# Optimization experiments

Hardware: AMD Instinct MI355X
Metric: run time of the kernel (lower is better)

## Reference

```python
import jax, jax.numpy as jnp
import numpy as np

N = 400000   # nnum_t (tokens)
C = 256      # dim
H = 8        # num_heads
HD = C // H  # head_dim = 32
K = 32       # patch_size
D = 4        # dilation
BLOCK = K * D
NA = ((N + BLOCK - 1) // BLOCK) * BLOCK  # nnum_a (padded length)
SCALE = HD ** -0.5
INVALID = -1000.0


def setup_inputs() -> dict:
    key = jax.random.key(0)
    ks = jax.random.split(key, 8)
    data = jax.random.normal(ks[0], (N, C), dtype=jnp.float32)
    xyz = jax.random.uniform(ks[1], (N, 3), dtype=jnp.float32) * 1024.0
    depth_idx = jnp.sort(jax.random.randint(ks[2], (N,), 0, 8)).astype(jnp.int64)
    Wqkv = jax.random.normal(ks[3], (C, 3 * C), dtype=jnp.float32) * 0.02
    bqkv = jnp.zeros((3 * C,), dtype=jnp.float32)
    Wproj = jax.random.normal(ks[4], (C, C), dtype=jnp.float32) * 0.02
    bproj = jnp.zeros((C,), dtype=jnp.float32)
    freqs = jax.random.normal(ks[5], (H, HD // 2, 3), dtype=jnp.float32) * 0.02
    return {"data": data, "xyz": xyz, "depth_idx": depth_idx,
            "Wqkv": Wqkv, "bqkv": bqkv, "Wproj": Wproj, "bproj": bproj,
            "freqs": freqs}


def _rotate_half(x):
    x1, x2 = jnp.split(x, 2, axis=-1)
    return jnp.concatenate([-x2, x1], axis=-1)


def reference(data, xyz, depth_idx, Wqkv, bqkv, Wproj, bproj, freqs):
    # qkv projection: (N, 3C)
    qkv = data @ Wqkv + bqkv
    qkv = qkv.reshape(N, 3, H, HD)

    # mixed RoPE: per-head learnable frequencies over 3D positions
    theta = jnp.einsum('nd,hfd->nhf', xyz, freqs)          # (N, H, HD/2)
    emb = jnp.concatenate([theta, theta], axis=-1)         # (N, H, HD)
    cos, sin = jnp.cos(emb), jnp.sin(emb)
    q = qkv[:, 0] * cos + _rotate_half(qkv[:, 0]) * sin
    k = qkv[:, 1] * cos + _rotate_half(qkv[:, 1]) * sin
    v = qkv[:, 2]
    qkv = jnp.stack([q, k, v], axis=1).reshape(N, 3 * C)

    # patch_partition: pad tokens to nnum_a
    pad = NA - N
    qkv = jnp.pad(qkv, ((0, pad), (0, 0)))
    max_d = depth_idx.max()
    depth_p = jnp.pad(depth_idx, (0, pad), constant_values=0) 
    if pad > 0:
        depth_p = depth_p.at[N:].set(max_d + 1)

    # dilation reshuffle: (-1, K, D, 3C) -> (-1, D, K, 3C) -> (-1, K, 3C)
    qkv = qkv.reshape(-1, K, D, 3 * C).transpose(0, 2, 1, 3).reshape(-1, K, 3 * C)
    # split heads: (B, H, K, HD) each
    qkv = qkv.reshape(-1, K, 3, H, HD).transpose(2, 0, 3, 1, 4)
    q, k, v = qkv[0], qkv[1], qkv[2]

    # teacher-forcing mask from depth indices (dilated layout, cond='le')
    m = depth_p.reshape(-1, K, D).transpose(0, 2, 1).reshape(-1, K)  # (B, K)
    diff = m[:, :, None] - m[:, None, :]
    mask = jnp.where(diff < 0, INVALID, 0.0).astype(jnp.float32)     # (B, K, K)

    # windowed attention
    scores = jnp.einsum('bhqd,bhkd->bhqk', q, k) * SCALE + mask[:, None]
    attn = jax.nn.softmax(scores, axis=-1)
    out = jnp.einsum('bhqk,bhkd->bhqd', attn, v)           # (B, H, K, HD)
    out = out.transpose(0, 2, 1, 3).reshape(-1, C)

    # reverse dilation reshuffle and unpad
    out = out.reshape(-1, D, K, C).transpose(0, 2, 1, 3).reshape(-1, C)
    out = out[:N]

    # output projection (dropout is identity at p=0 / eval)
    return out @ Wproj + bproj
```

## Files before the change

### kernel.cpp

```cpp
#include <hip/hip_runtime.h>
#include <math.h>


typedef float  float4v __attribute__((ext_vector_type(4)));
typedef short  bf16x8  __attribute__((ext_vector_type(8)));
typedef unsigned short us4 __attribute__((ext_vector_type(4)));

#define SCALE_ 0.17677669529663687f
#define INV2PI 0.15915494309189535f

__device__ __forceinline__ unsigned short f2bf(float x) {
  union { float f; unsigned u; } v; v.f = x;
  unsigned r = v.u + 0x7FFFu + ((v.u >> 16) & 1u);
  return (unsigned short)(r >> 16);
}
__device__ __forceinline__ unsigned pack2bf(float lo, float hi) {
  return (unsigned)f2bf(lo) | ((unsigned)f2bf(hi) << 16);
}
__device__ __forceinline__ float4v mfma16(bf16x8 a, bf16x8 b, float4v c) {
  return __builtin_amdgcn_mfma_f32_16x16x32_bf16(a, b, c, 0, 0, 0);
}
__device__ __forceinline__ int swz(int off) {
  return off ^ (((off >> 9) & 7) << 4);
}

__global__ __launch_bounds__(256) void k_prep(const float* __restrict__ wqkv,
                                              const float* __restrict__ wproj,
                                              unsigned short* __restrict__ wqf,
                                              unsigned short* __restrict__ wp) {
  int tid = blockIdx.x * 256 + threadIdx.x;
  if (tid < 768 * 256) {
    int h  = tid / 24576;
    int r  = tid - h * 24576;
    int mat = r >> 13;
    int r2  = r & 8191;
    int s = r2 >> 10, g = (r2 >> 8) & 3, col = (r2 >> 3) & 31, e = r2 & 7;
    int ci = s * 32 + g * 8 + e;
    int co = mat * 256 + h * 32 + col;
    wqf[tid] = f2bf(wqkv[ci * 768 + co]);
  } else {
    int u = tid - 768 * 256;
    int co = u >> 8, cpos = u & 255;
    int hh = cpos >> 5, ww = cpos & 31;
    int f = (ww & 1) ? 16 + (ww >> 1) : (ww >> 1);
    wp[u] = f2bf(wproj[(hh * 32 + f) * 256 + co]);
  }
}

#define K1_LDS_BYTES 81920

__global__ __launch_bounds__(512, 4) void k_fused(
    const float* __restrict__ data, const float* __restrict__ xyz,
    const int* __restrict__ depth, const float* __restrict__ bqkv,
    const float* __restrict__ freqs, const unsigned short* __restrict__ wqf,
    unsigned short* __restrict__ aout ) {
  extern __shared__ char smem[];
  const int b    = blockIdx.x;
  const int t    = threadIdx.x;
  const int lane = t & 63;
  const int w    = t >> 6;
  const int g    = lane >> 4;
  const int l15  = lane & 15;
  const int d    = w >> 1;
  const int half = w & 1;

  if (t < 128) ((int*)(smem + 78336))[t] =
      depth[b * 128 + ((t & 31) << 2) + (t >> 5)];
  if (t < 384) ((float*)(smem + 78848))[t] = xyz[(size_t)b * 384 + t];
  if (t < 384) ((float*)(smem + 80384))[t] = freqs[t];

  {
    const float* dbase = data + (size_t)b * 32768;
#pragma unroll
    for (int i = 0; i < 16; ++i) {
      const int fidx = i * 512 + t;
      const float4v v4 = *reinterpret_cast<const float4v*>(dbase + fidx * 4);
      us4 pk;
      pk.x = f2bf(v4.x); pk.y = f2bf(v4.y); pk.z = f2bf(v4.z); pk.w = f2bf(v4.w);
      *reinterpret_cast<us4*>(smem + swz(fidx * 8)) = pk;
    }
  }
  __syncthreads();

  bf16x8 areg[8];
#pragma unroll
  for (int s = 0; s < 8; ++s)
    areg[s] = *reinterpret_cast<const bf16x8*>(
        smem + swz((16 * w + l15) * 512 + s * 64 + g * 16));

  float maskf0[4], maskf1[4];
  {
    const int* ML = (const int*)(smem + 78336);
    const int mk0 = ML[32 * d + l15];
    const int mk1 = ML[32 * d + 16 + l15];
#pragma unroll
    for (int rr = 0; rr < 4; ++rr) {
      const int mq = ML[32 * d + 16 * half + 4 * g + rr];
      maskf0[rr] = (mq < mk0) ? -1000.f : 0.f;
      maskf1[rr] = (mq < mk1) ? -1000.f : 0.f;
    }
  }
  bf16x8 ones;
#pragma unroll
  for (int j = 0; j < 8; ++j) ones[j] = (short)0x3F80;

  __syncthreads();

  const int bb = g * 512 + l15 * 16;

#pragma unroll 1
  for (int h = 0; h < 8; ++h) {
    {
      const char* wb = (const char*)wqf + (size_t)h * 49152 + t * 16;
      const bf16x8 s0 = *reinterpret_cast<const bf16x8*>(wb);
      const bf16x8 s1 = *reinterpret_cast<const bf16x8*>(wb + 8192);
      const bf16x8 s2 = *reinterpret_cast<const bf16x8*>(wb + 16384);
      const bf16x8 s3 = *reinterpret_cast<const bf16x8*>(wb + 24576);
      const bf16x8 s4 = *reinterpret_cast<const bf16x8*>(wb + 32768);
      const bf16x8 s5 = *reinterpret_cast<const bf16x8*>(wb + 40960);
      char* wd = smem + t * 16;
      *reinterpret_cast<bf16x8*>(wd)         = s0;
      *reinterpret_cast<bf16x8*>(wd + 8192)  = s1;
      *reinterpret_cast<bf16x8*>(wd + 16384) = s2;
      *reinterpret_cast<bf16x8*>(wd + 24576) = s3;
      *reinterpret_cast<bf16x8*>(wd + 32768) = s4;
      *reinterpret_cast<bf16x8*>(wd + 40960) = s5;
    }
    __syncthreads();

    {
      float4v q0a = {0.f,0.f,0.f,0.f}, q1a = q0a, k0a = q0a, k1a = q0a;
#pragma unroll
      for (int s = 0; s < 8; ++s) {
        const bf16x8 bq0 = *reinterpret_cast<const bf16x8*>(smem + bb + s * 2048);
        const bf16x8 bq1 = *reinterpret_cast<const bf16x8*>(smem + bb + s * 2048 + 256);
        const bf16x8 bk0 = *reinterpret_cast<const bf16x8*>(smem + bb + s * 2048 + 16384);
        const bf16x8 bk1 = *reinterpret_cast<const bf16x8*>(smem + bb + s * 2048 + 16384 + 256);
        q0a = mfma16(areg[s], bq0, q0a);
        q1a = mfma16(areg[s], bq1, q1a);
        k0a = mfma16(areg[s], bk0, k0a);
        k1a = mfma16(areg[s], bk1, k1a);
      }
      const float bq0v = bqkv[h * 32 + l15];
      const float bq1v = bqkv[h * 32 + 16 + l15];
      const float bk0v = bqkv[256 + h * 32 + l15];
      const float bk1v = bqkv[256 + h * 32 + 16 + l15];
      const float* Fp = (const float*)(smem + 80384) + (h * 16 + l15) * 3;
      const float F0 = Fp[0], F1 = Fp[1], F2 = Fp[2];
#pragma unroll
      for (int rr = 0; rr < 4; ++rr) {
        const int row  = 16 * w + 4 * g + rr;
        const int prow = ((row & 3) << 5) | (row >> 2);
        const float* xp = (const float*)(smem + 78848) + row * 3;
        const float th = xp[0] * F0 + xp[1] * F1 + xp[2] * F2;
        float rev = th * INV2PI;
        rev -= floorf(rev);
        const float sn = __builtin_amdgcn_sinf(rev);
        const float cs = __builtin_amdgcn_cosf(rev);
        const float q0 = q0a[rr] + bq0v, q1 = q1a[rr] + bq1v;
        const float k0 = k0a[rr] + bk0v, k1 = k1a[rr] + bk1v;
        *reinterpret_cast<unsigned*>(smem + 49152 + prow * 80 + 4 * l15) =
            pack2bf(q0 * cs - q1 * sn, q1 * cs + q0 * sn);
        *reinterpret_cast<unsigned*>(smem + 59392 + prow * 80 + 4 * l15) =
            pack2bf(k0 * cs - k1 * sn, k1 * cs + k0 * sn);
      }
    }
    {
      float4v v0a = {0.f,0.f,0.f,0.f}, v1a = v0a;
#pragma unroll
      for (int s = 0; s < 8; ++s) {
        const bf16x8 bv0 = *reinterpret_cast<const bf16x8*>(smem + bb + s * 2048 + 32768);
        const bf16x8 bv1 = *reinterpret_cast<const bf16x8*>(smem + bb + s * 2048 + 32768 + 256);
        v0a = mfma16(areg[s], bv0, v0a);
        v1a = mfma16(areg[s], bv1, v1a);
      }
      const float bv0v = bqkv[512 + h * 32 + l15];
      const float bv1v = bqkv[512 + h * 32 + 16 + l15];
#pragma unroll
      for (int rr = 0; rr < 4; ++rr) {
        const int row = 16 * w + 4 * g + rr;
        const int kk = row >> 2, dd = row & 3;
        const int cpos = (kk < 16) ? (kk << 1) : (((kk - 16) << 1) | 1);
        *reinterpret_cast<unsigned short*>(
            smem + 69632 + l15 * 272 + (dd * 32 + cpos) * 2) = f2bf(v0a[rr] + bv0v);
        *reinterpret_cast<unsigned short*>(
            smem + 69632 + (l15 + 16) * 272 + (dd * 32 + cpos) * 2) = f2bf(v1a[rr] + bv1v);
      }
    }
    __syncthreads();

    {
      const bf16x8 aq = *reinterpret_cast<const bf16x8*>(
          smem + 49152 + (32 * d + 16 * half + l15) * 80 + 16 * g);
      const bf16x8 bk0 = *reinterpret_cast<const bf16x8*>(
          smem + 59392 + (32 * d + l15) * 80 + 16 * g);
      const bf16x8 bk1 = *reinterpret_cast<const bf16x8*>(
          smem + 59392 + (32 * d + 16 + l15) * 80 + 16 * g);
      float4v s0 = {0.f,0.f,0.f,0.f}, s1 = s0;
      s0 = mfma16(aq, bk0, s0);
      s1 = mfma16(aq, bk1, s1);

      char* plw = smem + w * 1280;
#pragma unroll
      for (int rr = 0; rr < 4; ++rr) {
        const float p0 = __expf(s0[rr] * SCALE_ + maskf0[rr]);
        const float p1 = __expf(s1[rr] * SCALE_ + maskf1[rr]);
        *reinterpret_cast<unsigned*>(plw + (4 * g + rr) * 80 + 4 * l15) =
            pack2bf(p0, p1);
      }
      const bf16x8 ap = *reinterpret_cast<const bf16x8*>(plw + l15 * 80 + 16 * g);
      const bf16x8 bv0 = *reinterpret_cast<const bf16x8*>(
          smem + 69632 + l15 * 272 + d * 64 + 16 * g);
      const bf16x8 bv1 = *reinterpret_cast<const bf16x8*>(
          smem + 69632 + (l15 + 16) * 272 + d * 64 + 16 * g);
      float4v o0 = {0.f,0.f,0.f,0.f}, o1 = o0, osum = o0;
      osum = mfma16(ap, ones, osum);
      o0   = mfma16(ap, bv0, o0);
      o1   = mfma16(ap, bv1, o1);

      char* ob = (char*)aout + (size_t)b * 131072 + h * 64;
#pragma unroll
      for (int rr = 0; rr < 4; ++rr) {
        const float rs = __builtin_amdgcn_rcpf(osum[rr]);
        const int n_local = (16 * half + 4 * g + rr) * 4 + d;
        *reinterpret_cast<unsigned*>(ob + n_local * 512 + 4 * l15) =
            pack2bf(o0[rr] * rs, o1[rr] * rs);
      }
    }
    __syncthreads();
  }
}

#define K2_LDS_BYTES 81920

__global__ __launch_bounds__(512, 4) void k_proj(
    const unsigned short* ain,
    const unsigned short* __restrict__ wproj_t,
    const float* __restrict__ bproj,
    float* out) {
  extern __shared__ char smem2[];
  const int b = blockIdx.x, t = threadIdx.x;
  const int lane = t & 63, w = t >> 6;
  const int g = lane >> 4, l15 = lane & 15;

  {
    const char* abase = (const char*)ain + (size_t)b * 131072;
    bf16x8 stg[8];
#pragma unroll
    for (int i = 0; i < 8; ++i)
      stg[i] = *reinterpret_cast<const bf16x8*>(abase + i * 8192 + t * 16);
#pragma unroll
    for (int i = 0; i < 8; ++i)
      *reinterpret_cast<bf16x8*>(smem2 + swz(i * 8192 + t * 16)) = stg[i];
  }
  __syncthreads();

  bf16x8 areg[8];
#pragma unroll
  for (int s = 0; s < 8; ++s)
    areg[s] = *reinterpret_cast<const bf16x8*>(
        smem2 + swz((16 * w + l15) * 512 + s * 64 + g * 16));

#pragma unroll 1
  for (int p = 0; p < 8; ++p) {
    const char* wb = (const char*)wproj_t + p * 16384;
    const bf16x8 s0 = *reinterpret_cast<const bf16x8*>(wb + t * 16);
    const bf16x8 s1 = *reinterpret_cast<const bf16x8*>(wb + 8192 + t * 16);
    __syncthreads();
    *reinterpret_cast<bf16x8*>(smem2 + 65536 + swz(t * 16)) = s0;
    *reinterpret_cast<bf16x8*>(smem2 + 65536 + swz(8192 + t * 16)) = s1;
    __syncthreads();

    float4v acc0 = {0.f,0.f,0.f,0.f}, acc1 = acc0;
#pragma unroll
    for (int s = 0; s < 8; ++s) {
      const int ko = s * 64 + g * 16;
      bf16x8 b0 = *reinterpret_cast<const bf16x8*>(smem2 + 65536 + swz(l15 * 512 + ko));
      bf16x8 b1 = *reinterpret_cast<const bf16x8*>(smem2 + 65536 + swz((l15 + 16) * 512 + ko));
      acc0 = mfma16(areg[s], b0, acc0);
      acc1 = mfma16(areg[s], b1, acc1);
    }
    const int col0 = 32 * p + l15, col1 = col0 + 16;
    const float bb0 = bproj[col0], bb1 = bproj[col1];
#pragma unroll
    for (int rr = 0; rr < 4; ++rr) {
      const int row = 16 * w + 4 * g + rr;
      out[((size_t)b * 128 + row) * 256 + col0] = acc0[rr] + bb0;
      out[((size_t)b * 128 + row) * 256 + col1] = acc1[rr] + bb1;
    }
  }
}

extern "C" void kernel_launch(void* const* d_in, const int* in_sizes, int n_in,
                              void* d_out, int out_size, void* d_ws, size_t ws_size,
                              hipStream_t stream) {
  const float* data  = (const float*)d_in[0];
  const float* xyz   = (const float*)d_in[1];
  const int*   depth = (const int*)d_in[2];
  const float* wqkv  = (const float*)d_in[3];
  const float* bqkv  = (const float*)d_in[4];
  const float* wproj = (const float*)d_in[5];
  const float* bproj = (const float*)d_in[6];
  const float* freqs = (const float*)d_in[7];

  unsigned short* wqkv_f  = (unsigned short*)d_ws;
  unsigned short* wproj_t = wqkv_f + 768 * 256;

  (void)hipFuncSetAttribute(reinterpret_cast<const void*>(k_fused),
                            hipFuncAttributeMaxDynamicSharedMemorySize, K1_LDS_BYTES);
  (void)hipFuncSetAttribute(reinterpret_cast<const void*>(k_proj),
                            hipFuncAttributeMaxDynamicSharedMemorySize, K2_LDS_BYTES);

  k_prep<<<dim3(1024), dim3(256), 0, stream>>>(wqkv, wproj, wqkv_f, wproj_t);
  k_fused<<<dim3(3125), dim3(512), K1_LDS_BYTES, stream>>>(
      data, xyz, depth, bqkv, freqs, wqkv_f, (unsigned short*)d_out);
  k_proj<<<dim3(3125), dim3(512), K2_LDS_BYTES, stream>>>(
      (const unsigned short*)d_out, wproj_t, bproj, (float*)d_out);
}
```

Baseline: 467.0 us.

## Retile per-head QKV GEMM so each wave covers 32 rows and split Q/K across waves

Changes the per-head QKV projection tiling. Each wave now holds A fragments for two 16-row M tiles and computes either Q or K (two N tiles) plus half of V, so every B fragment read from LDS feeds two MFMAs instead of one. It also folds the 1/(2π) factor into the freqs preload, uses the fract intrinsic for range reduction, and packs bf16 with the hardware v_cvt_pk_bf16_f32 instruction. The cost is double the A-fragment registers per wave, which may pressure occupancy under the 512x4 launch bounds.

```diff
diff --git a/kernel.cpp b/kernel.cpp
--- a/kernel.cpp
+++ b/kernel.cpp
@@ -16,6 +16,11 @@
 }
 __device__ __forceinline__ unsigned pack2bf(float lo, float hi) {
   return (unsigned)f2bf(lo) | ((unsigned)f2bf(hi) << 16);
+}
+__device__ __forceinline__ unsigned cvtpk(float lo, float hi) {
+  unsigned r;
+  asm("v_cvt_pk_bf16_f32 %0, %1, %2" : "=v"(r) : "v"(lo), "v"(hi));
+  return r;
 }
 __device__ __forceinline__ float4v mfma16(bf16x8 a, bf16x8 b, float4v c) {
   return __builtin_amdgcn_mfma_f32_16x16x32_bf16(a, b, c, 0, 0, 0);
@@ -59,15 +64,15 @@
   const int t    = threadIdx.x;
   const int lane = t & 63;
   const int w    = t >> 6;
+  const int wm   = w >> 1;
+  const int wn   = w & 1;
   const int g    = lane >> 4;
   const int l15  = lane & 15;
-  const int d    = w >> 1;
-  const int half = w & 1;
 
   if (t < 128) ((int*)(smem + 78336))[t] =
       depth[b * 128 + ((t & 31) << 2) + (t >> 5)];
   if (t < 384) ((float*)(smem + 78848))[t] = xyz[(size_t)b * 384 + t];
-  if (t < 384) ((float*)(smem + 80384))[t] = freqs[t];
+  if (t < 384) ((float*)(smem + 80384))[t] = freqs[t] * INV2PI;
 
   {
     const float* dbase = data + (size_t)b * 32768;
@@ -82,20 +87,22 @@
   }
   __syncthreads();
 
-  bf16x8 areg[8];
-#pragma unroll
-  for (int s = 0; s < 8; ++s)
-    areg[s] = *reinterpret_cast<const bf16x8*>(
-        smem + swz((16 * w + l15) * 512 + s * 64 + g * 16));
+  bf16x8 areg[2][8];
+#pragma unroll
+  for (int mt = 0; mt < 2; ++mt)
+#pragma unroll
+    for (int s = 0; s < 8; ++s)
+      areg[mt][s] = *reinterpret_cast<const bf16x8*>(
+          smem + swz((32 * wm + 16 * mt + l15) * 512 + s * 64 + g * 16));
 
   float maskf0[4], maskf1[4];
   {
     const int* ML = (const int*)(smem + 78336);
-    const int mk0 = ML[32 * d + l15];
-    const int mk1 = ML[32 * d + 16 + l15];
+    const int mk0 = ML[32 * wm + l15];
+    const int mk1 = ML[32 * wm + 16 + l15];
 #pragma unroll
     for (int rr = 0; rr < 4; ++rr) {
-      const int mq = ML[32 * d + 16 * half + 4 * g + rr];
+      const int mq = ML[32 * wm + 16 * wn + 4 * g + rr];
       maskf0[rr] = (mq < mk0) ? -1000.f : 0.f;
       maskf1[rr] = (mq < mk1) ? -1000.f : 0.f;
     }
@@ -106,7 +113,9 @@
 
   __syncthreads();
 
-  const int bb = g * 512 + l15 * 16;
+  const int bb    = g * 512 + l15 * 16;
+  const int mbase = wn ? 16384 : 0;
+  const int voff  = 32768 + (wn ? 256 : 0);
 
 #pragma unroll 1
   for (int h = 0; h < 8; ++h) {
@@ -128,74 +137,64 @@
     }
     __syncthreads();
 
+    float4v a0[2], a1[2], av[2];
+#pragma unroll
+    for (int mt = 0; mt < 2; ++mt) {
+      a0[mt] = (float4v){0.f, 0.f, 0.f, 0.f};
+      a1[mt] = a0[mt];
+      av[mt] = a0[mt];
+    }
+#pragma unroll
+    for (int s = 0; s < 8; ++s) {
+      const bf16x8 b0 = *reinterpret_cast<const bf16x8*>(smem + bb + s * 2048 + mbase);
+      const bf16x8 b1 = *reinterpret_cast<const bf16x8*>(smem + bb + s * 2048 + mbase + 256);
+      const bf16x8 bv = *reinterpret_cast<const bf16x8*>(smem + bb + s * 2048 + voff);
+#pragma unroll
+      for (int mt = 0; mt < 2; ++mt) {
+        a0[mt] = mfma16(areg[mt][s], b0, a0[mt]);
+        a1[mt] = mfma16(areg[mt][s], b1, a1[mt]);
+        av[mt] = mfma16(areg[mt][s], bv, av[mt]);
+      }
+    }
+
     {
-      float4v q0a = {0.f,0.f,0.f,0.f}, q1a = q0a, k0a = q0a, k1a = q0a;
-#pragma unroll
-      for (int s = 0; s < 8; ++s) {
-        const bf16x8 bq0 = *reinterpret_cast<const bf16x8*>(smem + bb + s * 2048);
-        const bf16x8 bq1 = *reinterpret_cast<const bf16x8*>(smem + bb + s * 2048 + 256);
-        const bf16x8 bk0 = *reinterpret_cast<const bf16x8*>(smem + bb + s * 2048 + 16384);
-        const bf16x8 bk1 = *reinterpret_cast<const bf16x8*>(smem + bb + s * 2048 + 16384 + 256);
-        q0a = mfma16(areg[s], bq0, q0a);
-        q1a = mfma16(areg[s], bq1, q1a);
-        k0a = mfma16(areg[s], bk0, k0a);
-        k1a = mfma16(areg[s], bk1, k1a);
-      }
-      const float bq0v = bqkv[h * 32 + l15];
-      const float bq1v = bqkv[h * 32 + 16 + l15];
-      const float bk0v = bqkv[256 + h * 32 + l15];
-      const float bk1v = bqkv[256 + h * 32 + 16 + l15];
+      const float bb0 = bqkv[wn * 256 + h * 32 + l15];
+      const float bb1 = bqkv[wn * 256 + h * 32 + 16 + l15];
+      const float bvv = bqkv[512 + h * 32 + 16 * wn + l15];
       const float* Fp = (const float*)(smem + 80384) + (h * 16 + l15) * 3;
       const float F0 = Fp[0], F1 = Fp[1], F2 = Fp[2];
-#pragma unroll
-      for (int rr = 0; rr < 4; ++rr) {
-        const int row  = 16 * w + 4 * g + rr;
-        const int prow = ((row & 3) << 5) | (row >> 2);
-        const float* xp = (const float*)(smem + 78848) + row * 3;
-        const float th = xp[0] * F0 + xp[1] * F1 + xp[2] * F2;
-        float rev = th * INV2PI;
-        rev -= floorf(rev);
-        const float sn = __builtin_amdgcn_sinf(rev);
-        const float cs = __builtin_amdgcn_cosf(rev);
-        const float q0 = q0a[rr] + bq0v, q1 = q1a[rr] + bq1v;
-        const float k0 = k0a[rr] + bk0v, k1 = k1a[rr] + bk1v;
-        *reinterpret_cast<unsigned*>(smem + 49152 + prow * 80 + 4 * l15) =
-            pack2bf(q0 * cs - q1 * sn, q1 * cs + q0 * sn);
-        *reinterpret_cast<unsigned*>(smem + 59392 + prow * 80 + 4 * l15) =
-            pack2bf(k0 * cs - k1 * sn, k1 * cs + k0 * sn);
-      }
-    }
-    {
-      float4v v0a = {0.f,0.f,0.f,0.f}, v1a = v0a;
-#pragma unroll
-      for (int s = 0; s < 8; ++s) {
-        const bf16x8 bv0 = *reinterpret_cast<const bf16x8*>(smem + bb + s * 2048 + 32768);
-        const bf16x8 bv1 = *reinterpret_cast<const bf16x8*>(smem + bb + s * 2048 + 32768 + 256);
-        v0a = mfma16(areg[s], bv0, v0a);
-        v1a = mfma16(areg[s], bv1, v1a);
-      }
-      const float bv0v = bqkv[512 + h * 32 + l15];
-      const float bv1v = bqkv[512 + h * 32 + 16 + l15];
-#pragma unroll
-      for (int rr = 0; rr < 4; ++rr) {
-        const int row = 16 * w + 4 * g + rr;
-        const int kk = row >> 2, dd = row & 3;
-        const int cpos = (kk < 16) ? (kk << 1) : (((kk - 16) << 1) | 1);
-        *reinterpret_cast<unsigned short*>(
-            smem + 69632 + l15 * 272 + (dd * 32 + cpos) * 2) = f2bf(v0a[rr] + bv0v);
-        *reinterpret_cast<unsigned short*>(
-            smem + 69632 + (l15 + 16) * 272 + (dd * 32 + cpos) * 2) = f2bf(v1a[rr] + bv1v);
-      }
+      char* qkdst = smem + (wn ? 59392 : 49152);
+      char* vdst  = smem + 69632 + (l15 + 16 * wn) * 272;
+#pragma unroll
+      for (int mt = 0; mt < 2; ++mt)
+#pragma unroll
+        for (int rr = 0; rr < 4; ++rr) {
+          const int row  = 32 * wm + 16 * mt + 4 * g + rr;
+          const int prow = ((row & 3) << 5) | (row >> 2);
+          const float* xp = (const float*)(smem + 78848) + row * 3;
+          const float th = xp[0] * F0 + xp[1] * F1 + xp[2] * F2;
+          const float fr = __builtin_amdgcn_fractf(th);
+          const float sn = __builtin_amdgcn_sinf(fr);
+          const float cs = __builtin_amdgcn_cosf(fr);
+          const float e0 = a0[mt][rr] + bb0;
+          const float e1 = a1[mt][rr] + bb1;
+          *reinterpret_cast<unsigned*>(qkdst + prow * 80 + 4 * l15) =
+              cvtpk(e0 * cs - e1 * sn, e1 * cs + e0 * sn);
+          const int kk = row >> 2, dd = row & 3;
+          const int cpos = (kk < 16) ? (kk << 1) : (((kk - 16) << 1) | 1);
+          *reinterpret_cast<unsigned short*>(vdst + (dd * 32 + cpos) * 2) =
+              f2bf(av[mt][rr] + bvv);
+        }
     }
     __syncthreads();
 
     {
       const bf16x8 aq = *reinterpret_cast<const bf16x8*>(
-          smem + 49152 + (32 * d + 16 * half + l15) * 80 + 16 * g);
+          smem + 49152 + (32 * wm + 16 * wn + l15) * 80 + 16 * g);
       const bf16x8 bk0 = *reinterpret_cast<const bf16x8*>(
-          smem + 59392 + (32 * d + l15) * 80 + 16 * g);
+          smem + 59392 + (32 * wm + l15) * 80 + 16 * g);
       const bf16x8 bk1 = *reinterpret_cast<const bf16x8*>(
-          smem + 59392 + (32 * d + 16 + l15) * 80 + 16 * g);
+          smem + 59392 + (32 * wm + 16 + l15) * 80 + 16 * g);
       float4v s0 = {0.f,0.f,0.f,0.f}, s1 = s0;
       s0 = mfma16(aq, bk0, s0);
       s1 = mfma16(aq, bk1, s1);
@@ -210,9 +209,9 @@
       }
       const bf16x8 ap = *reinterpret_cast<const bf16x8*>(plw + l15 * 80 + 16 * g);
       const bf16x8 bv0 = *reinterpret_cast<const bf16x8*>(
-          smem + 69632 + l15 * 272 + d * 64 + 16 * g);
+          smem + 69632 + l15 * 272 + wm * 64 + 16 * g);
       const bf16x8 bv1 = *reinterpret_cast<const bf16x8*>(
-          smem + 69632 + (l15 + 16) * 272 + d * 64 + 16 * g);
+          smem + 69632 + (l15 + 16) * 272 + wm * 64 + 16 * g);
       float4v o0 = {0.f,0.f,0.f,0.f}, o1 = o0, osum = o0;
       osum = mfma16(ap, ones, osum);
       o0   = mfma16(ap, bv0, o0);
@@ -222,7 +221,7 @@
 #pragma unroll
       for (int rr = 0; rr < 4; ++rr) {
         const float rs = __builtin_amdgcn_rcpf(osum[rr]);
-        const int n_local = (16 * half + 4 * g + rr) * 4 + d;
+        const int n_local = (16 * wn + 4 * g + rr) * 4 + wm;
         *reinterpret_cast<unsigned*>(ob + n_local * 512 + 4 * l15) =
             pack2bf(o0[rr] * rs, o1[rr] * rs);
       }
```

After: 636.4 us. 1.36x slower.

## Prefetch weights via direct global-to-LDS loads and overlap with compute

Applied to the files above, without the earlier changes.

Weight tiles in both the fused QKV/attention kernel and the projection kernel are now loaded with global_load_lds, which writes straight into shared memory without a register round trip. The next head's K/V weight slices and the next projection column block are prefetched during the current compute. The projection weights are also repacked into an MFMA-friendly layout so the swizzle is no longer needed. Smaller changes fold INV2PI into freqs, use a hardware fract in place of floor, and use a packed bf16 convert instruction. The trade-off is extra barriers and a dependence on async LDS-load ordering being correct.

```diff
diff --git a/kernel.cpp b/kernel.cpp
--- a/kernel.cpp
+++ b/kernel.cpp
@@ -17,17 +17,27 @@
 __device__ __forceinline__ unsigned pack2bf(float lo, float hi) {
   return (unsigned)f2bf(lo) | ((unsigned)f2bf(hi) << 16);
 }
+__device__ __forceinline__ unsigned cvtpk(float lo, float hi) {
+  unsigned r;
+  asm("v_cvt_pk_bf16_f32 %0, %1, %2" : "=v"(r) : "v"(lo), "v"(hi));
+  return r;
+}
 __device__ __forceinline__ float4v mfma16(bf16x8 a, bf16x8 b, float4v c) {
   return __builtin_amdgcn_mfma_f32_16x16x32_bf16(a, b, c, 0, 0, 0);
 }
 __device__ __forceinline__ int swz(int off) {
   return off ^ (((off >> 9) & 7) << 4);
+}
+__device__ __forceinline__ void gload16(const void* gsrc, char* ldst) {
+  __builtin_amdgcn_global_load_lds(
+      (const __attribute__((address_space(1))) unsigned int*)gsrc,
+      (__attribute__((address_space(3))) unsigned int*)ldst, 16, 0, 0);
 }
 
 __global__ __launch_bounds__(256) void k_prep(const float* __restrict__ wqkv,
                                               const float* __restrict__ wproj,
                                               unsigned short* __restrict__ wqf,
-                                              unsigned short* __restrict__ wp) {
+                                              unsigned short* __restrict__ wpf) {
   int tid = blockIdx.x * 256 + threadIdx.x;
   if (tid < 768 * 256) {
     int h  = tid / 24576;
@@ -40,10 +50,13 @@
     wqf[tid] = f2bf(wqkv[ci * 768 + co]);
   } else {
     int u = tid - 768 * 256;
-    int co = u >> 8, cpos = u & 255;
+    int p = u >> 13;
+    int r2 = u & 8191;
+    int s = r2 >> 10, g = (r2 >> 8) & 3, col = (r2 >> 3) & 31, e = r2 & 7;
+    int cpos = s * 32 + g * 8 + e;
     int hh = cpos >> 5, ww = cpos & 31;
     int f = (ww & 1) ? 16 + (ww >> 1) : (ww >> 1);
-    wp[u] = f2bf(wproj[(hh * 32 + f) * 256 + co]);
+    wpf[u] = f2bf(wproj[(hh * 32 + f) * 256 + p * 32 + col]);
   }
 }
 
@@ -67,7 +80,7 @@
   if (t < 128) ((int*)(smem + 78336))[t] =
       depth[b * 128 + ((t & 31) << 2) + (t >> 5)];
   if (t < 384) ((float*)(smem + 78848))[t] = xyz[(size_t)b * 384 + t];
-  if (t < 384) ((float*)(smem + 80384))[t] = freqs[t];
+  if (t < 384) ((float*)(smem + 80384))[t] = freqs[t] * INV2PI;
 
   {
     const float* dbase = data + (size_t)b * 32768;
@@ -106,25 +119,20 @@
 
   __syncthreads();
 
-  const int bb = g * 512 + l15 * 16;
+  const int wub    = (t >> 6) << 10;
+  const int bb     = g * 512 + l15 * 16;
+  const char* gblk = (const char*)wqf + t * 16;
+
+#pragma unroll
+  for (int j = 2; j < 6; ++j)
+    gload16(gblk + j * 8192, smem + j * 8192 + wub);
 
 #pragma unroll 1
   for (int h = 0; h < 8; ++h) {
     {
-      const char* wb = (const char*)wqf + (size_t)h * 49152 + t * 16;
-      const bf16x8 s0 = *reinterpret_cast<const bf16x8*>(wb);
-      const bf16x8 s1 = *reinterpret_cast<const bf16x8*>(wb + 8192);
-      const bf16x8 s2 = *reinterpret_cast<const bf16x8*>(wb + 16384);
-      const bf16x8 s3 = *reinterpret_cast<const bf16x8*>(wb + 24576);
-      const bf16x8 s4 = *reinterpret_cast<const bf16x8*>(wb + 32768);
-      const bf16x8 s5 = *reinterpret_cast<const bf16x8*>(wb + 40960);
-      char* wd = smem + t * 16;
-      *reinterpret_cast<bf16x8*>(wd)         = s0;
-      *reinterpret_cast<bf16x8*>(wd + 8192)  = s1;
-      *reinterpret_cast<bf16x8*>(wd + 16384) = s2;
-      *reinterpret_cast<bf16x8*>(wd + 24576) = s3;
-      *reinterpret_cast<bf16x8*>(wd + 32768) = s4;
-      *reinterpret_cast<bf16x8*>(wd + 40960) = s5;
+      const char* gh = gblk + (size_t)h * 49152;
+      gload16(gh, smem + wub);
+      gload16(gh + 8192, smem + 8192 + wub);
     }
     __syncthreads();
 
@@ -153,16 +161,15 @@
         const int prow = ((row & 3) << 5) | (row >> 2);
         const float* xp = (const float*)(smem + 78848) + row * 3;
         const float th = xp[0] * F0 + xp[1] * F1 + xp[2] * F2;
-        float rev = th * INV2PI;
-        rev -= floorf(rev);
-        const float sn = __builtin_amdgcn_sinf(rev);
-        const float cs = __builtin_amdgcn_cosf(rev);
+        const float fr = __builtin_amdgcn_fractf(th);
+        const float sn = __builtin_amdgcn_sinf(fr);
+        const float cs = __builtin_amdgcn_cosf(fr);
         const float q0 = q0a[rr] + bq0v, q1 = q1a[rr] + bq1v;
         const float k0 = k0a[rr] + bk0v, k1 = k1a[rr] + bk1v;
         *reinterpret_cast<unsigned*>(smem + 49152 + prow * 80 + 4 * l15) =
-            pack2bf(q0 * cs - q1 * sn, q1 * cs + q0 * sn);
+            cvtpk(q0 * cs - q1 * sn, q1 * cs + q0 * sn);
         *reinterpret_cast<unsigned*>(smem + 59392 + prow * 80 + 4 * l15) =
-            pack2bf(k0 * cs - k1 * sn, k1 * cs + k0 * sn);
+            cvtpk(k0 * cs - k1 * sn, k1 * cs + k0 * sn);
       }
     }
     {
@@ -188,6 +195,13 @@
       }
     }
     __syncthreads();
+
+    if (h < 7) {
+      const char* gn = gblk + (size_t)(h + 1) * 49152;
+#pragma unroll
+      for (int j = 2; j < 6; ++j)
+        gload16(gn + j * 8192, smem + j * 8192 + wub);
+    }
 
     {
       const bf16x8 aq = *reinterpret_cast<const bf16x8*>(
@@ -235,13 +249,15 @@
 
 __global__ __launch_bounds__(512, 4) void k_proj(
     const unsigned short* ain,
-    const unsigned short* __restrict__ wproj_t,
+    const unsigned short* __restrict__ wpf,
     const float* __restrict__ bproj,
     float* out) {
   extern __shared__ char smem2[];
   const int b = blockIdx.x, t = threadIdx.x;
   const int lane = t & 63, w = t >> 6;
   const int g = lane >> 4, l15 = lane & 15;
+  const int wub = (t >> 6) << 10;
+  const char* gblk = (const char*)wpf + t * 16;
 
   {
     const char* abase = (const char*)ain + (size_t)b * 131072;
@@ -253,6 +269,8 @@
     for (int i = 0; i < 8; ++i)
       *reinterpret_cast<bf16x8*>(smem2 + swz(i * 8192 + t * 16)) = stg[i];
   }
+  gload16(gblk, smem2 + 65536 + wub);
+  gload16(gblk + 8192, smem2 + 65536 + 8192 + wub);
   __syncthreads();
 
   bf16x8 areg[8];
@@ -263,22 +281,21 @@
 
 #pragma unroll 1
   for (int p = 0; p < 8; ++p) {
-    const char* wb = (const char*)wproj_t + p * 16384;
-    const bf16x8 s0 = *reinterpret_cast<const bf16x8*>(wb + t * 16);
-    const bf16x8 s1 = *reinterpret_cast<const bf16x8*>(wb + 8192 + t * 16);
-    __syncthreads();
-    *reinterpret_cast<bf16x8*>(smem2 + 65536 + swz(t * 16)) = s0;
-    *reinterpret_cast<bf16x8*>(smem2 + 65536 + swz(8192 + t * 16)) = s1;
-    __syncthreads();
-
     float4v acc0 = {0.f,0.f,0.f,0.f}, acc1 = acc0;
 #pragma unroll
     for (int s = 0; s < 8; ++s) {
-      const int ko = s * 64 + g * 16;
-      bf16x8 b0 = *reinterpret_cast<const bf16x8*>(smem2 + 65536 + swz(l15 * 512 + ko));
-      bf16x8 b1 = *reinterpret_cast<const bf16x8*>(smem2 + 65536 + swz((l15 + 16) * 512 + ko));
+      const bf16x8 b0 = *reinterpret_cast<const bf16x8*>(
+          smem2 + 65536 + s * 2048 + g * 512 + l15 * 16);
+      const bf16x8 b1 = *reinterpret_cast<const bf16x8*>(
+          smem2 + 65536 + s * 2048 + g * 512 + l15 * 16 + 256);
       acc0 = mfma16(areg[s], b0, acc0);
       acc1 = mfma16(areg[s], b1, acc1);
+    }
+    __syncthreads();
+    if (p < 7) {
+      const char* gn = gblk + (size_t)(p + 1) * 16384;
+      gload16(gn, smem2 + 65536 + wub);
+      gload16(gn + 8192, smem2 + 65536 + 8192 + wub);
     }
     const int col0 = 32 * p + l15, col1 = col0 + 16;
     const float bb0 = bproj[col0], bb1 = bproj[col1];
@@ -288,6 +305,7 @@
       out[((size_t)b * 128 + row) * 256 + col0] = acc0[rr] + bb0;
       out[((size_t)b * 128 + row) * 256 + col1] = acc1[rr] + bb1;
     }
+    __syncthreads();
   }
 }
 
@@ -304,16 +322,16 @@
   const float* freqs = (const float*)d_in[7];
 
   unsigned short* wqkv_f  = (unsigned short*)d_ws;
-  unsigned short* wproj_t = wqkv_f + 768 * 256;
+  unsigned short* wproj_f = wqkv_f + 768 * 256;
 
   (void)hipFuncSetAttribute(reinterpret_cast<const void*>(k_fused),
                             hipFuncAttributeMaxDynamicSharedMemorySize, K1_LDS_BYTES);
   (void)hipFuncSetAttribute(reinterpret_cast<const void*>(k_proj),
                             hipFuncAttributeMaxDynamicSharedMemorySize, K2_LDS_BYTES);
 
-  k_prep<<<dim3(1024), dim3(256), 0, stream>>>(wqkv, wproj, wqkv_f, wproj_t);
+  k_prep<<<dim3(1024), dim3(256), 0, stream>>>(wqkv, wproj, wqkv_f, wproj_f);
   k_fused<<<dim3(3125), dim3(512), K1_LDS_BYTES, stream>>>(
       data, xyz, depth, bqkv, freqs, wqkv_f, (unsigned short*)d_out);
   k_proj<<<dim3(3125), dim3(512), K2_LDS_BYTES, stream>>>(
-      (const unsigned short*)d_out, wproj_t, bproj, (float*)d_out);
-}
+      (const unsigned short*)d_out, wproj_f, bproj, (float*)d_out);
+}
```

After: 444.5 us. 4.8% less time.
